# Kernel optimization log

Measured on AMD Instinct MI355X. Metric: run time of the kernel, lower is better.

Reference implementation:

```python
import jax, jax.numpy as jnp
import numpy as np

N_NODES = 100000


def gcn_conv(x, W, b, src, dst, n_nodes):
    # PyG GCNConv: h = x @ W; add self-loops; norm = d^-1/2[src] * d^-1/2[dst];
    # aggregate sum of norm * h[src] at dst; then + bias.
    h = x @ W  # [N, F_out]
    loops = jnp.arange(n_nodes, dtype=src.dtype)
    s = jnp.concatenate([src, loops])  # [E+N]
    d = jnp.concatenate([dst, loops])
    deg = jax.ops.segment_sum(jnp.ones_like(d, dtype=h.dtype), d, num_segments=n_nodes)
    dinv = jax.lax.rsqrt(deg)  # deg >= 1 thanks to self-loops
    norm = dinv[s] * dinv[d]  # [E+N]
    msg = h[s] * norm[:, None]  # [E+N, F_out] -- large gather
    out = jax.ops.segment_sum(msg, d, num_segments=n_nodes)  # scatter-add
    return out + b


def setup_inputs() -> dict:
    key = jax.random.key(0)
    k = jax.random.split(key, 8)
    x = jax.random.normal(k[0], (N_NODES, 8), dtype=jnp.float32)
    edge_index = jax.random.randint(k[1], (2, 1600000), 0, N_NODES, dtype=jnp.int32)
    W1 = jax.random.normal(k[2], (8, 64), dtype=jnp.float32) * 0.3
    b1 = jnp.zeros((64,), dtype=jnp.float32)
    W2 = jax.random.normal(k[3], (64, 128), dtype=jnp.float32) * 0.1
    b2 = jnp.zeros((128,), dtype=jnp.float32)
    Wfc = jax.random.normal(k[4], (128, 1), dtype=jnp.float32) * 0.08
    bfc = jnp.zeros((1,), dtype=jnp.float32)
    return {"x": x, "edge_index": edge_index, "W1": W1, "b1": b1,
            "W2": W2, "b2": b2, "Wfc": Wfc, "bfc": bfc}


def reference(x, edge_index, W1, b1, W2, b2, Wfc, bfc):
    src, dst = edge_index[0], edge_index[1]
    n = x.shape[0]
    h = jax.nn.relu(gcn_conv(x, W1, b1, src, dst, n))   # dropout: eval mode (identity)
    h = jax.nn.relu(gcn_conv(h, W2, b2, src, dst, n))
    g = jnp.mean(h, axis=0)  # [128] graph readout
    return g @ Wfc + bfc     # [1]
```

## Files before the change

kernel.cpp:

```cpp
#include <hip/hip_runtime.h>


#define CHUNK 4096
#define NB_SHIFT 8
#define BCAP 5120
#define G2_GRID 1042

typedef float v2f __attribute__((ext_vector_type(2)));

__device__ __forceinline__ unsigned short f2bf(float f) {
    unsigned u = __float_as_uint(f);
    return (unsigned short)((u + 0x7fffu + ((u >> 16) & 1u)) >> 16);
}
__device__ __forceinline__ unsigned pkbf(float a, float b) {
    return ((unsigned)f2bf(b) << 16) | f2bf(a);
}
__device__ __forceinline__ float bflo(unsigned u) { return __uint_as_float(u << 16); }
__device__ __forceinline__ float bfhi(unsigned u) { return __uint_as_float(u & 0xffff0000u); }

__global__ void scatterA(const int* __restrict__ ei, int E, int* __restrict__ cursor,
                         unsigned int* __restrict__ bucketed) {
    __shared__ unsigned short bk[CHUNK];
    __shared__ unsigned int spk[CHUNK];
    __shared__ unsigned short sbk[CHUNK];
    __shared__ int h[512], hsc[512], lcur[512], rbase[512];
    int tid = threadIdx.x;
    h[tid] = 0;
    h[tid + 256] = 0;
    lcur[tid] = 0;
    lcur[tid + 256] = 0;
    __syncthreads();
    int cbase = blockIdx.x * CHUNK;
    int cN = min(CHUNK, E - cbase);
    const int* src = ei;
    const int* dst = ei + E;
    for (int i = tid; i < cN; i += 256) {
        int d = dst[cbase + i];
        int b = d >> NB_SHIFT;
        bk[i] = (unsigned short)b;
        atomicAdd(&h[b], 1);
    }
    __syncthreads();
    hsc[tid] = h[tid];
    hsc[tid + 256] = h[tid + 256];
    __syncthreads();
    for (int off = 1; off < 512; off <<= 1) {
        int v0 = (tid >= off) ? hsc[tid - off] : 0;
        int v1 = (tid + 256 >= off) ? hsc[tid + 256 - off] : 0;
        __syncthreads();
        hsc[tid] += v0;
        hsc[tid + 256] += v1;
        __syncthreads();
    }
    int ex0 = hsc[tid] - h[tid];
    int ex1 = hsc[tid + 256] - h[tid + 256];
    hsc[tid] = ex0;
    hsc[tid + 256] = ex1;
#pragma unroll
    for (int k = 0; k < 2; k++) {
        int i = tid + k * 256;
        if (h[i]) rbase[i] = i * BCAP + atomicAdd(&cursor[i], h[i]);
    }
    __syncthreads();
    for (int i = tid; i < cN; i += 256) {
        int s = src[cbase + i], d = dst[cbase + i];
        int b = bk[i];
        int pos = hsc[b] + atomicAdd(&lcur[b], 1);
        spk[pos] = (unsigned)s | ((unsigned)(d & 255) << 17);
        sbk[pos] = (unsigned short)b;
    }
    __syncthreads();
    for (int p = tid; p < cN; p += 256) {
        int b = sbk[p];
        bucketed[rbase[b] + (p - hsc[b])] = spk[p];
    }
}

__global__ void buildB(const unsigned int* __restrict__ bucketed,
                       const int* __restrict__ cursor, int* __restrict__ row_start,
                       int* __restrict__ cntg, float* __restrict__ dinv,
                       int* __restrict__ csr_src, const float* __restrict__ x,
                       unsigned int* __restrict__ xsb, int n) {
    __shared__ unsigned int spk[BCAP];
    __shared__ int scsr[BCAP];
    __shared__ int cnt[256], sc[256], cur[256];
    __shared__ float sdinv[256];
    int tid = threadIdx.x;
    int b = blockIdx.x;
    int s0 = b * BCAP;
    int m = cursor[b];
    cnt[tid] = 0;
    __syncthreads();
    for (int e = tid; e < m; e += 256) {
        unsigned v = bucketed[s0 + e];
        spk[e] = v;
        atomicAdd(&cnt[v >> 17], 1);
    }
    __syncthreads();
    sc[tid] = cnt[tid];
    __syncthreads();
    for (int off = 1; off < 256; off <<= 1) {
        int v0 = (tid >= off) ? sc[tid - off] : 0;
        __syncthreads();
        sc[tid] += v0;
        __syncthreads();
    }
    int nb0 = b << NB_SHIFT;
    int node = nb0 + tid;
    int ex = sc[tid] - cnt[tid];
    cur[tid] = ex;
    float dv = rsqrtf((float)cnt[tid] + 1.0f);
    sdinv[tid] = dv;
    if (node < n) {
        row_start[node] = s0 + ex;
        cntg[node] = cnt[tid];
        dinv[node] = dv;
    }
    __syncthreads();
    for (int e = tid; e < m; e += 256) {
        unsigned v = spk[e];
        int r = atomicAdd(&cur[v >> 17], 1);
        scsr[r] = (int)(v & 0x1FFFFu);
    }
    __syncthreads();
    for (int e = tid; e < m; e += 256) csr_src[s0 + e] = scsr[e];
    int lim = min(n - nb0, 256) * 4;
    for (int i = tid; i < lim; i += 256) {
        float2 v = ((const float2*)x)[nb0 * 4 + i];
        float dvv = sdinv[i >> 2];
        xsb[nb0 * 4 + i] = pkbf(v.x * dvv, v.y * dvv);
    }
}

__global__ __launch_bounds__(256) void aggX_gemm1(
    const unsigned int* __restrict__ xsb, const float* __restrict__ dinv,
    const int* __restrict__ row_start, const int* __restrict__ cnt,
    const int* __restrict__ csr_src, const float* __restrict__ W1,
    const float* __restrict__ b1, unsigned int* __restrict__ h1q, int n) {
    __shared__ float w[512 + 64];
    __shared__ float axl[64 * 8];
    __shared__ float sdi[64];
    int tid = threadIdx.x;
    for (int i = tid; i < 512; i += 256) w[i] = W1[i];
    if (tid < 64) w[512 + tid] = b1[tid];
    int g = tid >> 2, l = tid & 3;
    int node = blockIdx.x * 64 + g;
    float a[8] = {};
    float di = 0.f;
    if (node < n) {
        di = dinv[node];
        const uint4* xs4 = (const uint4*)xsb;
        int e0 = row_start[node], e1 = e0 + cnt[node];
        int e = e0 + l;
        for (; e + 4 < e1; e += 8) {
            int sA = csr_src[e], sB = csr_src[e + 4];
            uint4 uA = xs4[sA], uB = xs4[sB];
            a[0] += bflo(uA.x) + bflo(uB.x);
            a[1] += bfhi(uA.x) + bfhi(uB.x);
            a[2] += bflo(uA.y) + bflo(uB.y);
            a[3] += bfhi(uA.y) + bfhi(uB.y);
            a[4] += bflo(uA.z) + bflo(uB.z);
            a[5] += bfhi(uA.z) + bfhi(uB.z);
            a[6] += bflo(uA.w) + bflo(uB.w);
            a[7] += bfhi(uA.w) + bfhi(uB.w);
        }
        for (; e < e1; e += 4) {
            uint4 u = xs4[csr_src[e]];
            a[0] += bflo(u.x); a[1] += bfhi(u.x);
            a[2] += bflo(u.y); a[3] += bfhi(u.y);
            a[4] += bflo(u.z); a[5] += bfhi(u.z);
            a[6] += bflo(u.w); a[7] += bfhi(u.w);
        }
        if (l == 0) {
            uint4 u = xs4[node];
            a[0] += bflo(u.x); a[1] += bfhi(u.x);
            a[2] += bflo(u.y); a[3] += bfhi(u.y);
            a[4] += bflo(u.z); a[5] += bfhi(u.z);
            a[6] += bflo(u.w); a[7] += bfhi(u.w);
        }
    }
#pragma unroll
    for (int k = 0; k < 8; k++) {
        a[k] += __shfl_xor(a[k], 1);
        a[k] += __shfl_xor(a[k], 2);
    }
    axl[g * 8 + 2 * l] = di * a[2 * l];
    axl[g * 8 + 2 * l + 1] = di * a[2 * l + 1];
    if (l == 0) sdi[g] = di;
    __syncthreads();
    int wv = tid >> 6, lane = tid & 63;
    int nb = blockIdx.x * 64;
    for (int it = 0; it < 16; it++) {
        int nl = wv * 16 + it;
        int nd = nb + nl;
        if (nd >= n) break;
        float h = w[512 + lane];
#pragma unroll
        for (int k = 0; k < 8; k++) h = fmaf(axl[nl * 8 + k], w[k * 64 + lane], h);
        float h1s = fmaxf(h, 0.f) * sdi[nl];
        unsigned word = ((unsigned)__builtin_amdgcn_cvt_pk_fp8_f32(h1s, h1s, 0, false)
                         & 0xFFu) << ((lane & 3) * 8);
        word |= __shfl_xor((int)word, 1);
        word |= __shfl_xor((int)word, 2);
        if ((lane & 3) == 0) h1q[nd * 16 + (lane >> 2)] = word;
    }
}

__global__ void agg64(const unsigned int* __restrict__ h1q, const float* __restrict__ dinv,
                      const int* __restrict__ row_start, const int* __restrict__ cnt,
                      const int* __restrict__ csr_src, uint2* __restrict__ ahb, int n) {
    int gid = blockIdx.x * blockDim.x + threadIdx.x;
    int node = gid >> 4;
    if (node >= n) return;
    int cq = threadIdx.x & 15;
    int es = cq >> 2, qp = cq & 3;
    const uint4* h4 = (const uint4*)h1q;
    float a[16] = {};
    int e0 = row_start[node], e1 = e0 + cnt[node];
    int e = e0 + es;
    for (; e + 4 < e1; e += 8) {
        int sA = csr_src[e], sB = csr_src[e + 4];
        uint4 uA = h4[sA * 4 + qp], uB = h4[sB * 4 + qp];
#pragma unroll
        for (int wdx = 0; wdx < 4; wdx++) {
            unsigned wa = (&uA.x)[wdx], wb = (&uB.x)[wdx];
            v2f la = __builtin_amdgcn_cvt_pk_f32_fp8((int)wa, false);
            v2f ha = __builtin_amdgcn_cvt_pk_f32_fp8((int)wa, true);
            v2f lb = __builtin_amdgcn_cvt_pk_f32_fp8((int)wb, false);
            v2f hb = __builtin_amdgcn_cvt_pk_f32_fp8((int)wb, true);
            a[wdx * 4 + 0] += la[0] + lb[0];
            a[wdx * 4 + 1] += la[1] + lb[1];
            a[wdx * 4 + 2] += ha[0] + hb[0];
            a[wdx * 4 + 3] += ha[1] + hb[1];
        }
    }
    for (; e < e1; e += 4) {
        uint4 u = h4[csr_src[e] * 4 + qp];
#pragma unroll
        for (int wdx = 0; wdx < 4; wdx++) {
            unsigned wu = (&u.x)[wdx];
            v2f lo = __builtin_amdgcn_cvt_pk_f32_fp8((int)wu, false);
            v2f hi = __builtin_amdgcn_cvt_pk_f32_fp8((int)wu, true);
            a[wdx * 4 + 0] += lo[0];
            a[wdx * 4 + 1] += lo[1];
            a[wdx * 4 + 2] += hi[0];
            a[wdx * 4 + 3] += hi[1];
        }
    }
    if (es == 0) {
        uint4 u = h4[node * 4 + qp];
#pragma unroll
        for (int wdx = 0; wdx < 4; wdx++) {
            unsigned wu = (&u.x)[wdx];
            v2f lo = __builtin_amdgcn_cvt_pk_f32_fp8((int)wu, false);
            v2f hi = __builtin_amdgcn_cvt_pk_f32_fp8((int)wu, true);
            a[wdx * 4 + 0] += lo[0];
            a[wdx * 4 + 1] += lo[1];
            a[wdx * 4 + 2] += hi[0];
            a[wdx * 4 + 3] += hi[1];
        }
    }
#pragma unroll
    for (int k = 0; k < 16; k++) {
        a[k] += __shfl_xor(a[k], 4);
        a[k] += __shfl_xor(a[k], 8);
    }
    if (es == 0) {
        float di = dinv[node];
        uint4 r0, r1;
        r0.x = pkbf(di * a[0], di * a[1]);
        r0.y = pkbf(di * a[2], di * a[3]);
        r0.z = pkbf(di * a[4], di * a[5]);
        r0.w = pkbf(di * a[6], di * a[7]);
        r1.x = pkbf(di * a[8], di * a[9]);
        r1.y = pkbf(di * a[10], di * a[11]);
        r1.z = pkbf(di * a[12], di * a[13]);
        r1.w = pkbf(di * a[14], di * a[15]);
        uint4* out4 = (uint4*)ahb;
        out4[node * 8 + qp * 2] = r0;
        out4[node * 8 + qp * 2 + 1] = r1;
    }
}

__global__ __launch_bounds__(256) void gemm2_fused(
    const uint2* __restrict__ ahb, const float* __restrict__ W2,
    const float* __restrict__ b2, float* __restrict__ partial, int n) {
    __shared__ float w[64 * 128];
    __shared__ float at[32 * 64];
    __shared__ float csum[8 * 128];
    int tid = threadIdx.x;
    for (int i = tid; i < 64 * 128; i += 256) w[i] = W2[i];
    int ng = tid >> 5;
    int cg = tid & 31;
    int c0 = cg * 4;
    float b_0 = b2[c0], b_1 = b2[c0 + 1], b_2 = b2[c0 + 2], b_3 = b2[c0 + 3];
    float col0 = 0.f, col1 = 0.f, col2 = 0.f, col3 = 0.f;
    int ntiles = (n + 31) >> 5;
    for (int t = blockIdx.x; t < ntiles; t += gridDim.x) {
        int base = t * 32;
        __syncthreads();
        for (int i = tid; i < 512; i += 256) {
            int node = base + (i >> 4);
            int q = i & 15;
            uint2 v = (node < n) ? ahb[node * 16 + q] : make_uint2(0u, 0u);
            at[(i >> 4) * 64 + q * 4]     = bflo(v.x);
            at[(i >> 4) * 64 + q * 4 + 1] = bfhi(v.x);
            at[(i >> 4) * 64 + q * 4 + 2] = bflo(v.y);
            at[(i >> 4) * 64 + q * 4 + 3] = bfhi(v.y);
        }
        __syncthreads();
        float acc[4][4] = {};
        for (int kk = 0; kk < 64; kk += 4) {
            float ar[4][4], wr[4][4];
#pragma unroll
            for (int i = 0; i < 4; i++)
#pragma unroll
                for (int k = 0; k < 4; k++) ar[i][k] = at[(ng * 4 + i) * 64 + kk + k];
#pragma unroll
            for (int k = 0; k < 4; k++)
#pragma unroll
                for (int j = 0; j < 4; j++) wr[k][j] = w[(kk + k) * 128 + c0 + j];
#pragma unroll
            for (int i = 0; i < 4; i++)
#pragma unroll
                for (int j = 0; j < 4; j++)
#pragma unroll
                    for (int k = 0; k < 4; k++)
                        acc[i][j] = fmaf(ar[i][k], wr[k][j], acc[i][j]);
        }
        int nvalid = n - base;
#pragma unroll
        for (int i = 0; i < 4; i++) {
            if (ng * 4 + i < nvalid) {
                col0 += fmaxf(acc[i][0] + b_0, 0.f);
                col1 += fmaxf(acc[i][1] + b_1, 0.f);
                col2 += fmaxf(acc[i][2] + b_2, 0.f);
                col3 += fmaxf(acc[i][3] + b_3, 0.f);
            }
        }
    }
    csum[ng * 128 + c0] = col0;
    csum[ng * 128 + c0 + 1] = col1;
    csum[ng * 128 + c0 + 2] = col2;
    csum[ng * 128 + c0 + 3] = col3;
    __syncthreads();
    if (tid < 128) {
        float s = 0.f;
#pragma unroll
        for (int g = 0; g < 8; g++) s += csum[g * 128 + tid];
        partial[blockIdx.x * 128 + tid] = s;
    }
}

__global__ __launch_bounds__(1024) void finish_kernel(
    const float* __restrict__ partial, const float* __restrict__ Wfc,
    const float* __restrict__ bfc, float* __restrict__ out, float invN) {
    __shared__ float sh[1024 + 2];
    int tid = threadIdx.x;
    int c = tid & 127, g = tid >> 7;
    float s = 0.f;
#pragma unroll 8
    for (int b = g; b < G2_GRID; b += 8) s += partial[b * 128 + c];
    sh[tid] = s;
    __syncthreads();
    if (tid < 512) sh[tid] += sh[tid + 512];
    __syncthreads();
    if (tid < 256) sh[tid] += sh[tid + 256];
    __syncthreads();
    if (tid < 128) {
        float v = (sh[tid] + sh[tid + 128]) * Wfc[tid];
#pragma unroll
        for (int off = 32; off > 0; off >>= 1) v += __shfl_down(v, off);
        if ((tid & 63) == 0) sh[1024 + (tid >> 6)] = v;
    }
    __syncthreads();
    if (tid == 0) out[0] = (sh[1024] + sh[1025]) * invN + bfc[0];
}

extern "C" void kernel_launch(void* const* d_in, const int* in_sizes, int n_in,
                              void* d_out, int out_size, void* d_ws, size_t ws_size,
                              hipStream_t stream) {
    const float* x   = (const float*)d_in[0];
    const int* ei    = (const int*)d_in[1];
    const float* W1  = (const float*)d_in[2];
    const float* b1  = (const float*)d_in[3];
    const float* W2  = (const float*)d_in[4];
    const float* b2  = (const float*)d_in[5];
    const float* Wfc = (const float*)d_in[6];
    const float* bfc = (const float*)d_in[7];
    float* out = (float*)d_out;

    const int n = in_sizes[0] / 8;
    const int E = in_sizes[1] / 2;

    const int nA = (E + CHUNK - 1) / CHUNK;
    const int B = (n + 255) >> NB_SHIFT;

    char* ws = (char*)d_ws;
    size_t off = 0;
    auto alloc = [&](size_t bytes) -> char* {
        char* p = ws + off;
        off = (off + bytes + 255) & ~(size_t)255;
        return p;
    };
    int*            cursor    = (int*)alloc(512 * 4);
    unsigned int*   bucketed  = (unsigned int*)alloc((size_t)B * BCAP * 4);
    int*            row_start = (int*)alloc((size_t)n * 4);
    int*            cnt       = (int*)alloc((size_t)n * 4);
    float*          dinv      = (float*)alloc((size_t)n * 4);
    int*            csr_src   = (int*)alloc((size_t)B * BCAP * 4);
    unsigned int*   xsb       = (unsigned int*)alloc((size_t)n * 16);
    unsigned int*   h1q       = (unsigned int*)alloc((size_t)n * 64);
    uint2*          ahb       = (uint2*)alloc((size_t)n * 128);
    float*          partial   = (float*)alloc((size_t)G2_GRID * 128 * 4);
    (void)ws_size;

    hipMemsetAsync(cursor, 0, 512 * 4, stream);
    scatterA<<<nA, 256, 0, stream>>>(ei, E, cursor, bucketed);
    buildB<<<B, 256, 0, stream>>>(bucketed, cursor, row_start, cnt, dinv, csr_src,
                                  x, xsb, n);
    aggX_gemm1<<<(n + 63) / 64, 256, 0, stream>>>(xsb, dinv, row_start, cnt, csr_src,
                                                  W1, b1, h1q, n);
    agg64<<<(n * 16 + 255) / 256, 256, 0, stream>>>(h1q, dinv, row_start, cnt, csr_src,
                                                    ahb, n);
    gemm2_fused<<<G2_GRID, 256, 0, stream>>>(ahb, W2, b2, partial, n);
    finish_kernel<<<1, 1024, 0, stream>>>(partial, Wfc, bfc, out, 1.0f / (float)n);
}
```

Measured before the change: 189.5 us.

## Fuse final reduction into gemm2, pack bf16 operands in LDS, cache packed edges

The separate finish kernel is folded into gemm2_fused: the last block to arrive, found through an atomic counter on an unused cursor slot, reduces the per-block partials and writes the output. This removes one kernel launch. gemm2 now keeps W2 and the activation tile as packed bf16 pairs in shared memory and loads them as vectors, which cuts LDS footprint and load count but rounds W2 to bf16. scatterA packs each edge into shared memory in its first pass, so the second pass no longer re-reads src and dst from global memory.

```diff
diff --git a/kernel.cpp b/kernel.cpp
--- a/kernel.cpp
+++ b/kernel.cpp
@@ -20,6 +20,7 @@
 
 __global__ void scatterA(const int* __restrict__ ei, int E, int* __restrict__ cursor,
                          unsigned int* __restrict__ bucketed) {
+    __shared__ unsigned int pk[CHUNK];
     __shared__ unsigned short bk[CHUNK];
     __shared__ unsigned int spk[CHUNK];
     __shared__ unsigned short sbk[CHUNK];
@@ -35,8 +36,9 @@
     const int* src = ei;
     const int* dst = ei + E;
     for (int i = tid; i < cN; i += 256) {
-        int d = dst[cbase + i];
+        int s = src[cbase + i], d = dst[cbase + i];
         int b = d >> NB_SHIFT;
+        pk[i] = (unsigned)s | ((unsigned)(d & 255) << 17);
         bk[i] = (unsigned short)b;
         atomicAdd(&h[b], 1);
     }
@@ -52,10 +54,8 @@
         hsc[tid + 256] += v1;
         __syncthreads();
     }
-    int ex0 = hsc[tid] - h[tid];
-    int ex1 = hsc[tid + 256] - h[tid + 256];
-    hsc[tid] = ex0;
-    hsc[tid + 256] = ex1;
+    hsc[tid] -= h[tid];
+    hsc[tid + 256] -= h[tid + 256];
 #pragma unroll
     for (int k = 0; k < 2; k++) {
         int i = tid + k * 256;
@@ -63,10 +63,9 @@
     }
     __syncthreads();
     for (int i = tid; i < cN; i += 256) {
-        int s = src[cbase + i], d = dst[cbase + i];
         int b = bk[i];
         int pos = hsc[b] + atomicAdd(&lcur[b], 1);
-        spk[pos] = (unsigned)s | ((unsigned)(d & 255) << 17);
+        spk[pos] = pk[i];
         sbk[pos] = (unsigned short)b;
     }
     __syncthreads();
@@ -284,12 +283,18 @@
 
 __global__ __launch_bounds__(256) void gemm2_fused(
     const uint2* __restrict__ ahb, const float* __restrict__ W2,
-    const float* __restrict__ b2, float* __restrict__ partial, int n) {
-    __shared__ float w[64 * 128];
-    __shared__ float at[32 * 64];
+    const float* __restrict__ b2, float* __restrict__ partial,
+    const float* __restrict__ Wfc, const float* __restrict__ bfc,
+    float* __restrict__ out, int* __restrict__ done, float invN, int n) {
+    __shared__ __align__(16) unsigned wp[32 * 128];
+    __shared__ __align__(16) unsigned atp[32 * 32];
     __shared__ float csum[8 * 128];
+    __shared__ int lastFlag;
     int tid = threadIdx.x;
-    for (int i = tid; i < 64 * 128; i += 256) w[i] = W2[i];
+    for (int i = tid; i < 32 * 128; i += 256) {
+        int kp = i >> 7, j = i & 127;
+        wp[i] = pkbf(W2[(2 * kp) * 128 + j], W2[(2 * kp + 1) * 128 + j]);
+    }
     int ng = tid >> 5;
     int cg = tid & 31;
     int c0 = cg * 4;
@@ -301,32 +306,39 @@
         __syncthreads();
         for (int i = tid; i < 512; i += 256) {
             int node = base + (i >> 4);
-            int q = i & 15;
-            uint2 v = (node < n) ? ahb[node * 16 + q] : make_uint2(0u, 0u);
-            at[(i >> 4) * 64 + q * 4]     = bflo(v.x);
-            at[(i >> 4) * 64 + q * 4 + 1] = bfhi(v.x);
-            at[(i >> 4) * 64 + q * 4 + 2] = bflo(v.y);
-            at[(i >> 4) * 64 + q * 4 + 3] = bfhi(v.y);
+            uint2 v = (node < n) ? ahb[node * 16 + (i & 15)] : make_uint2(0u, 0u);
+            ((uint2*)atp)[i] = v;
         }
         __syncthreads();
         float acc[4][4] = {};
-        for (int kk = 0; kk < 64; kk += 4) {
-            float ar[4][4], wr[4][4];
-#pragma unroll
-            for (int i = 0; i < 4; i++)
-#pragma unroll
-                for (int k = 0; k < 4; k++) ar[i][k] = at[(ng * 4 + i) * 64 + kk + k];
-#pragma unroll
-            for (int k = 0; k < 4; k++)
-#pragma unroll
-                for (int j = 0; j < 4; j++) wr[k][j] = w[(kk + k) * 128 + c0 + j];
-#pragma unroll
-            for (int i = 0; i < 4; i++)
-#pragma unroll
-                for (int j = 0; j < 4; j++)
-#pragma unroll
-                    for (int k = 0; k < 4; k++)
-                        acc[i][j] = fmaf(ar[i][k], wr[k][j], acc[i][j]);
+        for (int kp = 0; kp < 32; kp += 4) {
+            uint4 ar0 = *(const uint4*)&atp[(ng * 4 + 0) * 32 + kp];
+            uint4 ar1 = *(const uint4*)&atp[(ng * 4 + 1) * 32 + kp];
+            uint4 ar2 = *(const uint4*)&atp[(ng * 4 + 2) * 32 + kp];
+            uint4 ar3 = *(const uint4*)&atp[(ng * 4 + 3) * 32 + kp];
+#pragma unroll
+            for (int k = 0; k < 4; k++) {
+                uint4 wv = *(const uint4*)&wp[(kp + k) * 128 + c0];
+                float wl0 = bflo(wv.x), wh0 = bfhi(wv.x);
+                float wl1 = bflo(wv.y), wh1 = bfhi(wv.y);
+                float wl2 = bflo(wv.z), wh2 = bfhi(wv.z);
+                float wl3 = bflo(wv.w), wh3 = bfhi(wv.w);
+                unsigned a0 = (&ar0.x)[k], a1 = (&ar1.x)[k];
+                unsigned a2 = (&ar2.x)[k], a3 = (&ar3.x)[k];
+#define GSTEP(I, AV)                                                        \
+                {                                                           \
+                    float al = bflo(AV), ah = bfhi(AV);                     \
+                    acc[I][0] = fmaf(al, wl0, fmaf(ah, wh0, acc[I][0]));    \
+                    acc[I][1] = fmaf(al, wl1, fmaf(ah, wh1, acc[I][1]));    \
+                    acc[I][2] = fmaf(al, wl2, fmaf(ah, wh2, acc[I][2]));    \
+                    acc[I][3] = fmaf(al, wl3, fmaf(ah, wh3, acc[I][3]));    \
+                }
+                GSTEP(0, a0)
+                GSTEP(1, a1)
+                GSTEP(2, a2)
+                GSTEP(3, a3)
+#undef GSTEP
+            }
         }
         int nvalid = n - base;
 #pragma unroll
@@ -350,31 +362,28 @@
         for (int g = 0; g < 8; g++) s += csum[g * 128 + tid];
         partial[blockIdx.x * 128 + tid] = s;
     }
-}
-
-__global__ __launch_bounds__(1024) void finish_kernel(
-    const float* __restrict__ partial, const float* __restrict__ Wfc,
-    const float* __restrict__ bfc, float* __restrict__ out, float invN) {
-    __shared__ float sh[1024 + 2];
-    int tid = threadIdx.x;
+    __threadfence();
+    __syncthreads();
+    if (tid == 0) lastFlag = (atomicAdd(done, 1) == (int)gridDim.x - 1);
+    __syncthreads();
+    if (!lastFlag) return;
+    __threadfence();
     int c = tid & 127, g = tid >> 7;
     float s = 0.f;
-#pragma unroll 8
-    for (int b = g; b < G2_GRID; b += 8) s += partial[b * 128 + c];
-    sh[tid] = s;
-    __syncthreads();
-    if (tid < 512) sh[tid] += sh[tid + 512];
-    __syncthreads();
-    if (tid < 256) sh[tid] += sh[tid + 256];
+    int G = gridDim.x;
+#pragma unroll 4
+    for (int b = g; b < G; b += 2) s += partial[b * 128 + c];
+    __syncthreads();
+    csum[g * 128 + c] = s;
     __syncthreads();
     if (tid < 128) {
-        float v = (sh[tid] + sh[tid + 128]) * Wfc[tid];
+        float v = (csum[tid] + csum[128 + tid]) * Wfc[tid];
 #pragma unroll
         for (int off = 32; off > 0; off >>= 1) v += __shfl_down(v, off);
-        if ((tid & 63) == 0) sh[1024 + (tid >> 6)] = v;
-    }
-    __syncthreads();
-    if (tid == 0) out[0] = (sh[1024] + sh[1025]) * invN + bfc[0];
+        if ((tid & 63) == 0) csum[256 + (tid >> 6)] = v;
+    }
+    __syncthreads();
+    if (tid == 0) out[0] = (csum[256] + csum[257]) * invN + bfc[0];
 }
 
 extern "C" void kernel_launch(void* const* d_in, const int* in_sizes, int n_in,
@@ -423,6 +432,6 @@
                                                   W1, b1, h1q, n);
     agg64<<<(n * 16 + 255) / 256, 256, 0, stream>>>(h1q, dinv, row_start, cnt, csr_src,
                                                     ahb, n);
-    gemm2_fused<<<G2_GRID, 256, 0, stream>>>(ahb, W2, b2, partial, n);
-    finish_kernel<<<1, 1024, 0, stream>>>(partial, Wfc, bfc, out, 1.0f / (float)n);
-}
+    gemm2_fused<<<G2_GRID, 256, 0, stream>>>(ahb, W2, b2, partial, Wfc, bfc, out,
+                                             &cursor[511], 1.0f / (float)n, n);
+}
```

New measurement: 286.9 us. +51.4%, slower.
